# Kernel tuning notes

Measured on AMD Instinct MI355X. Metric: run time of the kernel, lower is better.

## Reference

```python
import jax, jax.numpy as jnp
import numpy as np

N_HEADS = 16
D_HEAD = 64
TAU = 30.0
NEG = -1e9


def setup_inputs() -> dict:
    key = jax.random.key(0)
    k1, k2, k3, k4 = jax.random.split(key, 4)
    B, L, D = 2, 2048, 1024
    scale = 1.0 / np.sqrt(D)
    return {
        "input": jax.random.normal(k1, (B, L, D), dtype=jnp.float32),
        "attention_mask": jnp.ones((B, L), dtype=jnp.int32),
        "W_Q": jax.random.normal(k2, (N_HEADS * D_HEAD, D), dtype=jnp.float32) * scale,
        "W_K": jax.random.normal(k3, (N_HEADS * D_HEAD, D), dtype=jnp.float32) * scale,
        "W_V": jax.random.normal(k4, (N_HEADS * D_HEAD, D), dtype=jnp.float32) * scale,
    }


def reference(input, attention_mask, W_Q, W_K, W_V):
    B, L, D = input.shape
    # fused QKV projection (F.linear: x @ W.T), split into heads: [B, H, L, Dh]
    def proj(W):
        return jnp.einsum('bld,ed->ble', input, W).reshape(B, L, N_HEADS, D_HEAD).transpose(0, 2, 1, 3)
    q, k, v = proj(W_Q), proj(W_K), proj(W_V)
    S = jnp.einsum('bhqd,bhkd->bhqk', q, k) / np.sqrt(D_HEAD)  # [B,H,L,L]
    S = TAU * jnp.tanh(S)
    causal = jnp.tril(jnp.ones((L, L), dtype=bool))            # True = keep
    keep = causal[None, None, :, :] & (attention_mask[:, None, None, :] != 0)
    S = jnp.where(keep, S, NEG)
    attn = jax.nn.softmax(S, axis=-1)
    out = jnp.einsum('bhqk,bhkd->bhqd', attn, v)
    return out.transpose(0, 2, 1, 3).reshape(B, L, N_HEADS * D_HEAD)
```

## Files before the change

kernel.cpp:

```cpp
#include <hip/hip_runtime.h>
#include <hip/hip_bf16.h>


typedef unsigned short u16;
typedef __bf16 bf16x8 __attribute__((ext_vector_type(8)));
typedef float f32x4 __attribute__((ext_vector_type(4)));

#define MFMA(a, b, c) __builtin_amdgcn_mfma_f32_16x16x32_bf16(a, b, c, 0, 0, 0)

__device__ __forceinline__ u16 bf16rne(float f) {
    unsigned int u = __float_as_uint(f);
    u += 0x7fffu + ((u >> 16) & 1u);
    return (u16)(u >> 16);
}
__device__ __forceinline__ float bf16f(u16 h) {
    return __uint_as_float(((unsigned int)h) << 16);
}
__device__ __forceinline__ void split1(float f, u16& hi, u16& lo) {
    hi = bf16rne(f);
    lo = bf16rne(f - bf16f(hi));
}
__device__ __forceinline__ unsigned int pk2(float a, float b) {
    __hip_bfloat162 t = __float22bfloat162_rn(float2{a, b});
    return *(unsigned int*)&t;
}

__device__ __forceinline__ void gl16(const u16* g, u16* l) {
    __builtin_amdgcn_global_load_lds(
        (const __attribute__((address_space(1))) unsigned int*)g,
        (__attribute__((address_space(3))) unsigned int*)l, 16, 0, 0);
}

__global__ __launch_bounds__(256) void presplit(
    const float* __restrict__ X, const float* __restrict__ Wq,
    const float* __restrict__ Wk, const float* __restrict__ Wv,
    u16* __restrict__ Xh, u16* __restrict__ Xl,
    u16* __restrict__ Wqh, u16* __restrict__ Wql,
    u16* __restrict__ Wkh, u16* __restrict__ Wkl,
    u16* __restrict__ Wvh)
{
    int i = blockIdx.x * 256 + threadIdx.x;
    const float* src; u16 *dh, *dl; int off;
    if (i < 1048576)      { src = X;  dh = Xh;  dl = Xl;      off = i; }
    else if (i < 1310720) { src = Wq; dh = Wqh; dl = Wql;     off = i - 1048576; }
    else if (i < 1572864) { src = Wk; dh = Wkh; dl = Wkl;     off = i - 1310720; }
    else                  { src = Wv; dh = Wvh; dl = nullptr; off = i - 1572864; }
    float4 v = ((const float4*)src)[off];
    ushort4 h, l;
    split1(v.x, h.x, l.x); split1(v.y, h.y, l.y);
    split1(v.z, h.z, l.z); split1(v.w, h.w, l.w);
    ((ushort4*)dh)[off] = h;
    if (dl) ((ushort4*)dl)[off] = l;
}

__global__ __launch_bounds__(256, 4) void qkv_gemm(
    const u16* __restrict__ Xh, const u16* __restrict__ Xl,
    const u16* __restrict__ Wqh, const u16* __restrict__ Wql,
    const u16* __restrict__ Wkh, const u16* __restrict__ Wkl,
    const u16* __restrict__ Wvh,
    u16* __restrict__ Qh, u16* __restrict__ Ql,
    u16* __restrict__ Kh, u16* __restrict__ Kl,
    u16* __restrict__ VT)
{
    __shared__ __align__(16) u16 S[16384];
    u16* const Xhs = &S[0];
    u16* const Xls = &S[4096];
    u16* const Whs = &S[8192];
    u16* const Wls = &S[12288];
    const int tid = threadIdx.x;
    const int wave = tid >> 6, lane = tid & 63, quad = lane >> 4, c16 = lane & 15;
    const int id = blockIdx.x;
    const int nb = (((id >> 3) % 3) << 3) | (id & 7);
    const int m0 = ((id >> 3) / 3) * 128;
    const int mat = nb >> 3;
    const int n0 = (nb & 7) * 128;
    const u16* Bh = (mat == 0) ? Wqh : ((mat == 1) ? Wkh : Wvh);
    const u16* Bl = (mat == 0) ? Wql : Wkl;
    const int nseg = (mat < 2) ? 3 : 1;
    const int wm = (wave >> 1) * 64, wn = (wave & 1) * 64;

    const int srow0 = wave * 32 + (lane >> 2), scol = (lane & 3) * 8;

    f32x4 acc[4][4];
#pragma unroll
    for (int i = 0; i < 4; i++)
#pragma unroll
        for (int j = 0; j < 4; j++) acc[i][j] = (f32x4){0.f, 0.f, 0.f, 0.f};

    for (int kt = 0; kt < 32; kt++) {
        const int kcol = kt * 32;
#pragma unroll
        for (int s = 0; s < 2; s++) {
            int row = srow0 + s * 16;
            size_t go = (size_t)row * 1024 + kcol + scol;
            int lo = row * 32 + scol;
            gl16(Xh + (size_t)m0 * 1024 + go, &Xhs[lo]);
            gl16(Bh + (size_t)n0 * 1024 + go, &Whs[lo]);
            if (nseg == 3) {
                gl16(Xl + (size_t)m0 * 1024 + go, &Xls[lo]);
                gl16(Bl + (size_t)n0 * 1024 + go, &Wls[lo]);
            }
        }
        __syncthreads();
        for (int seg = 0; seg < nseg; seg++) {
            const u16* ap = (seg < 2) ? Xhs : Xls;
            const u16* bp = (seg == 1) ? Wls : Whs;
            bf16x8 af[4], bfr[4];
#pragma unroll
            for (int mt = 0; mt < 4; mt++)
                af[mt] = *(const bf16x8*)&ap[(wm + mt * 16 + c16) * 32 + quad * 8];
#pragma unroll
            for (int nt = 0; nt < 4; nt++)
                bfr[nt] = *(const bf16x8*)&bp[(wn + nt * 16 + c16) * 32 + quad * 8];
#pragma unroll
            for (int mt = 0; mt < 4; mt++)
#pragma unroll
                for (int nt = 0; nt < 4; nt++)
                    acc[mt][nt] = MFMA(af[mt], bfr[nt], acc[mt][nt]);
        }
        __syncthreads();
    }

    if (mat == 2) {
        u16* const T2 = &S[wave * 4096];
        const int nglob = n0 + wn + lane;
        const int hh = nglob >> 6, dh = nglob & 63;
        const int bh64 = ((m0 >> 11) * 16 + hh) * 64 + dh;
        u16* const vrow = VT + (size_t)bh64 * 2048 + (m0 & 2047) + wm;
#pragma unroll
        for (int half = 0; half < 2; half++) {
#pragma unroll
            for (int mt2 = 0; mt2 < 2; mt2++) {
                int mt = half * 2 + mt2;
#pragma unroll
                for (int nt = 0; nt < 4; nt++) {
                    uint2 d;
                    d.x = pk2(acc[mt][nt][0], acc[mt][nt][1]);
                    d.y = pk2(acc[mt][nt][2], acc[mt][nt][3]);
                    *(uint2*)&T2[(nt * 16 + c16) * 40 + mt2 * 16 + quad * 4] = d;
                }
            }
#pragma unroll
            for (int c = 0; c < 4; c++) {
                uint4 d = *(const uint4*)&T2[lane * 40 + c * 8];
                *(uint4*)&vrow[half * 32 + c * 8] = d;
            }
        }
    } else {
        const float scale = (mat == 0) ? 0.125f : 1.f;
#pragma unroll
        for (int mt = 0; mt < 4; mt++) {
#pragma unroll
            for (int nt = 0; nt < 4; nt++) {
#pragma unroll
                for (int reg = 0; reg < 4; reg++) {
                    int mm = m0 + wm + mt * 16 + quad * 4 + reg;
                    int n = n0 + wn + nt * 16 + c16;
                    int b_ = mm >> 11, l = mm & 2047;
                    int h = n >> 6, dh = n & 63;
                    float v = acc[mt][nt][reg] * scale;
                    u16 hi, lo; split1(v, hi, lo);
                    int idx = ((b_ * 16 + h) * 2048 + l) * 64 + dh;
                    if (mat == 0) { Qh[idx] = hi; Ql[idx] = lo; }
                    else          { Kh[idx] = hi; Kl[idx] = lo; }
                }
            }
        }
    }
}

__global__ __launch_bounds__(256, 4) void attn(
    const u16* __restrict__ Qh, const u16* __restrict__ Ql,
    const u16* __restrict__ Kh, const u16* __restrict__ Kl,
    const u16* __restrict__ VT, const int* __restrict__ AM,
    u16* __restrict__ Op, float* __restrict__ Lp)
{
    __shared__ __align__(16) u16 Khs[2][4096];
    __shared__ __align__(16) u16 Kls[2][4096];
    __shared__ __align__(16) u16 Ps[4096];

    const int tid = threadIdx.x, wave = tid >> 6, lane = tid & 63;
    const int quad = lane >> 4, c16 = lane & 15;
    const int bh = blockIdx.x;
    const int pr = blockIdx.y;
    const int sp = blockIdx.z;
    const int b_ = bh >> 4;
    const size_t base = (size_t)bh * 2048 * 64;

    const int swsub[2] = { (wave * 2) >> 2, (wave * 2 + 1) >> 2 };
    const int swrow[2] = { ((wave * 2) & 3) * 16 + (lane >> 2), ((wave * 2 + 1) & 3) * 16 + (lane >> 2) };
    const int scol = (lane & 3) * 8;

    auto stageK = [&](int k0, int buf) {
        const u16* Kht = Kh + base + (size_t)k0 * 64;
        const u16* Klt = Kl + base + (size_t)k0 * 64;
#pragma unroll
        for (int s = 0; s < 2; s++) {
            int sub = swsub[s], row = swrow[s];
            int lo = sub * 2048 + row * 32 + scol;
            gl16(Kht + (size_t)row * 64 + sub * 32 + scol, &Khs[buf][lo]);
            gl16(Klt + (size_t)row * 64 + sub * 32 + scol, &Kls[buf][lo]);
        }
    };

    for (int tix = 0; tix < 2; ++tix) {
        const int qt = tix ? pr : 31 - pr;
        const int q0 = qt * 64;

        const size_t qrow = base + (size_t)(q0 + wave * 16 + c16) * 64 + quad * 8;
        bf16x8 qh0 = *(const bf16x8*)&Qh[qrow];
        bf16x8 qh1 = *(const bf16x8*)&Qh[qrow + 32];
        bf16x8 ql0 = *(const bf16x8*)&Ql[qrow];
        bf16x8 ql1 = *(const bf16x8*)&Ql[qrow + 32];

        float rsl[4] = {0.f, 0.f, 0.f, 0.f};
        f32x4 o[4];
#pragma unroll
        for (int r = 0; r < 4; r++) o[r] = (f32x4){0.f, 0.f, 0.f, 0.f};

        if (sp <= qt) {
            stageK(sp * 64, 0);
            int cur = 0;
            for (int kb = sp; kb <= qt; kb += 2) {
                const int k0 = kb * 64;
                __syncthreads();
                if (kb + 2 <= qt) stageK(k0 + 128, cur ^ 1);

                int mk[4];
#pragma unroll
                for (int nt = 0; nt < 4; nt++)
                    mk[nt] = AM[b_ * 2048 + k0 + nt * 16 + c16];
                bf16x8 vf[4][2];
#pragma unroll
                for (int dt = 0; dt < 4; dt++) {
                    const size_t vrow = (size_t)(bh * 64 + dt * 16 + c16) * 2048 + k0 + quad * 8;
                    vf[dt][0] = *(const bf16x8*)&VT[vrow];
                    vf[dt][1] = *(const bf16x8*)&VT[vrow + 32];
                }
                const bool interior = (kb < qt);

                float p[4][4];
#pragma unroll
                for (int nt = 0; nt < 4; nt++) {
                    bf16x8 kh0 = *(const bf16x8*)&Khs[cur][(nt * 16 + c16) * 32 + quad * 8];
                    bf16x8 kh1 = *(const bf16x8*)&Khs[cur][2048 + (nt * 16 + c16) * 32 + quad * 8];
                    bf16x8 kl0 = *(const bf16x8*)&Kls[cur][(nt * 16 + c16) * 32 + quad * 8];
                    bf16x8 kl1 = *(const bf16x8*)&Kls[cur][2048 + (nt * 16 + c16) * 32 + quad * 8];
                    f32x4 sa = (f32x4){0.f, 0.f, 0.f, 0.f};
                    sa = MFMA(qh0, kh0, sa);
                    sa = MFMA(qh1, kh1, sa);
                    sa = MFMA(ql0, kh0, sa);
                    sa = MFMA(ql1, kh1, sa);
                    sa = MFMA(qh0, kl0, sa);
                    sa = MFMA(qh1, kl1, sa);
                    const int key = k0 + nt * 16 + c16;
                    const bool mok = (mk[nt] != 0);
#pragma unroll
                    for (int reg = 0; reg < 4; reg++) {
                        int qg = q0 + wave * 16 + quad * 4 + reg;
                        float x = sa[reg];
                        float e1 = __expf(2.f * x);
                        float r  = __builtin_amdgcn_rcpf(e1 + 1.f);
                        float pv = __expf(-60.f * r);
                        bool keep = mok && (interior || key <= qg);
                        pv = keep ? pv : 0.f;
                        p[nt][reg] = pv;
                        rsl[reg] += pv;
                    }
                }

#pragma unroll
                for (int nt = 0; nt < 4; nt++) {
                    int kl_ = nt * 16 + c16, sub = kl_ >> 5, kc = kl_ & 31;
#pragma unroll
                    for (int reg = 0; reg < 4; reg++)
                        Ps[sub * 2048 + (wave * 16 + quad * 4 + reg) * 32 + kc] = bf16rne(p[nt][reg]);
                }
                bf16x8 p0 = *(const bf16x8*)&Ps[(wave * 16 + c16) * 32 + quad * 8];
                bf16x8 p1 = *(const bf16x8*)&Ps[2048 + (wave * 16 + c16) * 32 + quad * 8];
#pragma unroll
                for (int dt = 0; dt < 4; dt++) {
                    o[dt] = MFMA(p0, vf[dt][0], o[dt]);
                    o[dt] = MFMA(p1, vf[dt][1], o[dt]);
                }
                cur ^= 1;
            }
        }
        __syncthreads();

        const size_t obase = (((size_t)sp * 1024 + (size_t)bh * 32 + qt) * 4096);
        const size_t lbase = (((size_t)sp * 1024 + (size_t)bh * 32 + qt) * 64);
        float lsum[4];
#pragma unroll
        for (int reg = 0; reg < 4; reg++) {
            float v = rsl[reg];
#pragma unroll
            for (int off = 1; off < 16; off <<= 1)
                v += __shfl_xor(v, off);
            lsum[reg] = v;
        }
        if (c16 == 0) {
#pragma unroll
            for (int reg = 0; reg < 4; reg++)
                Lp[lbase + wave * 16 + quad * 4 + reg] = lsum[reg];
        }
#pragma unroll
        for (int dt = 0; dt < 4; dt++)
#pragma unroll
            for (int reg = 0; reg < 4; reg++) {
                int row = wave * 16 + quad * 4 + reg;
                int d = dt * 16 + c16;
                Op[obase + row * 64 + d] = bf16rne(o[dt][reg]);
            }
    }
}

__global__ __launch_bounds__(256) void combine(
    const u16* __restrict__ Op, const float* __restrict__ Lp,
    float* __restrict__ Out)
{
    const int i = blockIdx.x * 256 + threadIdx.x;
    const size_t lin = (size_t)i * 4;
    const int d  = (int)(lin & 1023);
    const int h  = d >> 6, dd = d & 63;
    const int l  = (int)((lin >> 10) & 2047);
    const int b  = (int)(lin >> 21);
    const int qt = l >> 6, row = l & 63;
    const int bh = b * 16 + h;
    const size_t o0 = (((size_t)bh * 32 + qt) * 4096) + row * 64 + dd;
    const size_t o1 = o0 + (size_t)1024 * 4096;
    const size_t l0 = (((size_t)bh * 32 + qt) * 64) + row;
    ushort4 pa = *(const ushort4*)&Op[o0];
    ushort4 pb = *(const ushort4*)&Op[o1];
    float inv = __builtin_amdgcn_rcpf(Lp[l0] + Lp[l0 + 65536]);
    float4 r;
    r.x = (bf16f(pa.x) + bf16f(pb.x)) * inv;
    r.y = (bf16f(pa.y) + bf16f(pb.y)) * inv;
    r.z = (bf16f(pa.z) + bf16f(pb.z)) * inv;
    r.w = (bf16f(pa.w) + bf16f(pb.w)) * inv;
    *(float4*)&Out[lin] = r;
}

extern "C" void kernel_launch(void* const* d_in, const int* in_sizes, int n_in,
                              void* d_out, int out_size, void* d_ws, size_t ws_size,
                              hipStream_t stream) {
    const float* X  = (const float*)d_in[0];
    const int*   AM = (const int*)d_in[1];
    const float* Wq = (const float*)d_in[2];
    const float* Wk = (const float*)d_in[3];
    const float* Wv = (const float*)d_in[4];
    float* out = (float*)d_out;

    const size_t NE = (size_t)2 * 16 * 2048 * 64;
    const size_t WN = (size_t)1024 * 1024;
    u16* Qh  = (u16*)d_ws;
    u16* Ql  = Qh + NE;
    u16* Kh  = Ql + NE;
    u16* Kl  = Kh + NE;
    u16* VT  = Kl + NE;
    u16* Xh  = VT + NE;
    u16* Xl  = Xh + NE;
    u16* Wqh = Xl + NE;
    u16* Wql = Wqh + WN;
    u16* Wkh = Wql + WN;
    u16* Wkl = Wkh + WN;
    u16* Wvh = Wkl + WN;
    u16*   Op = Xh;
    float* Lp = (float*)Wqh;

    presplit<<<7168, 256, 0, stream>>>(X, Wq, Wk, Wv, Xh, Xl, Wqh, Wql, Wkh, Wkl, Wvh);
    qkv_gemm<<<768, 256, 0, stream>>>(Xh, Xl, Wqh, Wql, Wkh, Wkl, Wvh,
                                      Qh, Ql, Kh, Kl, VT);
    attn<<<dim3(32, 16, 2), 256, 0, stream>>>(Qh, Ql, Kh, Kl, VT, AM, Op, Lp);
    combine<<<4096, 256, 0, stream>>>(Op, Lp, out);
}
```

Measured before the change: 242.7 us.

## Transpose QK^T MFMA so P stays in registers and skip LDS round-trip

The attention kernel swaps the MFMA operand order so each lane holds scores for one query across four consecutive keys. That lets the P tile be packed straight into bf16x8 registers for the PV MFMA, removing the Ps shared-memory write/read and the per-row 16-lane shuffle reduction. V loads are split into two 4-element halves to match the new key ordering. The exponentials now use exp2 with log2e folded into the Q scale and the tanh constant, and the mask is read as int4. The QKV GEMM reorders its split-bf16 MFMA segments to reuse loaded fragments and lowers its occupancy hint from 4 to 3, which changes the register budget.

```diff
diff --git a/kernel.cpp b/kernel.cpp
--- a/kernel.cpp
+++ b/kernel.cpp
@@ -4,6 +4,7 @@
 
 typedef unsigned short u16;
 typedef __bf16 bf16x8 __attribute__((ext_vector_type(8)));
+typedef __bf16 bf16x4 __attribute__((ext_vector_type(4)));
 typedef float f32x4 __attribute__((ext_vector_type(4)));
 
 #define MFMA(a, b, c) __builtin_amdgcn_mfma_f32_16x16x32_bf16(a, b, c, 0, 0, 0)
@@ -23,6 +24,13 @@
 __device__ __forceinline__ unsigned int pk2(float a, float b) {
     __hip_bfloat162 t = __float22bfloat162_rn(float2{a, b});
     return *(unsigned int*)&t;
+}
+__device__ __forceinline__ float fexp2(float x) {
+#if __has_builtin(__builtin_amdgcn_exp2f)
+    return __builtin_amdgcn_exp2f(x);
+#else
+    return __expf(x * 0.6931471805599453f);
+#endif
 }
 
 __device__ __forceinline__ void gl16(const u16* g, u16* l) {
@@ -53,7 +61,7 @@
     if (dl) ((ushort4*)dl)[off] = l;
 }
 
-__global__ __launch_bounds__(256, 4) void qkv_gemm(
+__global__ __launch_bounds__(256, 3) void qkv_gemm(
     const u16* __restrict__ Xh, const u16* __restrict__ Xl,
     const u16* __restrict__ Wqh, const u16* __restrict__ Wql,
     const u16* __restrict__ Wkh, const u16* __restrict__ Wkl,
@@ -102,21 +110,37 @@
             }
         }
         __syncthreads();
-        for (int seg = 0; seg < nseg; seg++) {
-            const u16* ap = (seg < 2) ? Xhs : Xls;
-            const u16* bp = (seg == 1) ? Wls : Whs;
-            bf16x8 af[4], bfr[4];
+        bf16x8 xh[4], wh[4];
+#pragma unroll
+        for (int mt = 0; mt < 4; mt++)
+            xh[mt] = *(const bf16x8*)&Xhs[(wm + mt * 16 + c16) * 32 + quad * 8];
+#pragma unroll
+        for (int nt = 0; nt < 4; nt++)
+            wh[nt] = *(const bf16x8*)&Whs[(wn + nt * 16 + c16) * 32 + quad * 8];
+#pragma unroll
+        for (int mt = 0; mt < 4; mt++)
+#pragma unroll
+            for (int nt = 0; nt < 4; nt++)
+                acc[mt][nt] = MFMA(xh[mt], wh[nt], acc[mt][nt]);
+        if (nseg == 3) {
+            bf16x8 wl[4];
+#pragma unroll
+            for (int nt = 0; nt < 4; nt++)
+                wl[nt] = *(const bf16x8*)&Wls[(wn + nt * 16 + c16) * 32 + quad * 8];
 #pragma unroll
             for (int mt = 0; mt < 4; mt++)
-                af[mt] = *(const bf16x8*)&ap[(wm + mt * 16 + c16) * 32 + quad * 8];
-#pragma unroll
-            for (int nt = 0; nt < 4; nt++)
-                bfr[nt] = *(const bf16x8*)&bp[(wn + nt * 16 + c16) * 32 + quad * 8];
+#pragma unroll
+                for (int nt = 0; nt < 4; nt++)
+                    acc[mt][nt] = MFMA(xh[mt], wl[nt], acc[mt][nt]);
+            bf16x8 xl[4];
 #pragma unroll
             for (int mt = 0; mt < 4; mt++)
+                xl[mt] = *(const bf16x8*)&Xls[(wm + mt * 16 + c16) * 32 + quad * 8];
+#pragma unroll
+            for (int mt = 0; mt < 4; mt++)
 #pragma unroll
                 for (int nt = 0; nt < 4; nt++)
-                    acc[mt][nt] = MFMA(af[mt], bfr[nt], acc[mt][nt]);
+                    acc[mt][nt] = MFMA(xl[mt], wh[nt], acc[mt][nt]);
         }
         __syncthreads();
     }
@@ -147,7 +171,7 @@
             }
         }
     } else {
-        const float scale = (mat == 0) ? 0.125f : 1.f;
+        const float scale = (mat == 0) ? 0.36067376022224085f : 1.f;
 #pragma unroll
         for (int mt = 0; mt < 4; mt++) {
 #pragma unroll
@@ -177,7 +201,6 @@
 {
     __shared__ __align__(16) u16 Khs[2][4096];
     __shared__ __align__(16) u16 Kls[2][4096];
-    __shared__ __align__(16) u16 Ps[4096];
 
     const int tid = threadIdx.x, wave = tid >> 6, lane = tid & 63;
     const int quad = lane >> 4, c16 = lane & 15;
@@ -203,6 +226,8 @@
         }
     };
 
+    union U8 { uint4 u; bf16x8 v; };
+
     for (int tix = 0; tix < 2; ++tix) {
         const int qt = tix ? pr : 31 - pr;
         const int q0 = qt * 64;
@@ -213,7 +238,7 @@
         bf16x8 ql0 = *(const bf16x8*)&Ql[qrow];
         bf16x8 ql1 = *(const bf16x8*)&Ql[qrow + 32];
 
-        float rsl[4] = {0.f, 0.f, 0.f, 0.f};
+        float rsl = 0.f;
         f32x4 o[4];
 #pragma unroll
         for (int r = 0; r < 4; r++) o[r] = (f32x4){0.f, 0.f, 0.f, 0.f};
@@ -221,21 +246,26 @@
         if (sp <= qt) {
             stageK(sp * 64, 0);
             int cur = 0;
+            const int qg = q0 + wave * 16 + c16;
             for (int kb = sp; kb <= qt; kb += 2) {
                 const int k0 = kb * 64;
                 __syncthreads();
                 if (kb + 2 <= qt) stageK(k0 + 128, cur ^ 1);
 
-                int mk[4];
+                int4 mk[4];
 #pragma unroll
                 for (int nt = 0; nt < 4; nt++)
-                    mk[nt] = AM[b_ * 2048 + k0 + nt * 16 + c16];
-                bf16x8 vf[4][2];
+                    mk[nt] = *(const int4*)&AM[b_ * 2048 + k0 + nt * 16 + quad * 4];
+                bf16x4 vlo[4][2], vhi[4][2];
 #pragma unroll
                 for (int dt = 0; dt < 4; dt++) {
-                    const size_t vrow = (size_t)(bh * 64 + dt * 16 + c16) * 2048 + k0 + quad * 8;
-                    vf[dt][0] = *(const bf16x8*)&VT[vrow];
-                    vf[dt][1] = *(const bf16x8*)&VT[vrow + 32];
+#pragma unroll
+                    for (int hf = 0; hf < 2; hf++) {
+                        const size_t vb = (size_t)(bh * 64 + dt * 16 + c16) * 2048
+                                        + k0 + hf * 32 + quad * 4;
+                        vlo[dt][hf] = *(const bf16x4*)&VT[vb];
+                        vhi[dt][hf] = *(const bf16x4*)&VT[vb + 16];
+                    }
                 }
                 const bool interior = (kb < qt);
 
@@ -247,41 +277,39 @@
                     bf16x8 kl0 = *(const bf16x8*)&Kls[cur][(nt * 16 + c16) * 32 + quad * 8];
                     bf16x8 kl1 = *(const bf16x8*)&Kls[cur][2048 + (nt * 16 + c16) * 32 + quad * 8];
                     f32x4 sa = (f32x4){0.f, 0.f, 0.f, 0.f};
-                    sa = MFMA(qh0, kh0, sa);
-                    sa = MFMA(qh1, kh1, sa);
-                    sa = MFMA(ql0, kh0, sa);
-                    sa = MFMA(ql1, kh1, sa);
-                    sa = MFMA(qh0, kl0, sa);
-                    sa = MFMA(qh1, kl1, sa);
-                    const int key = k0 + nt * 16 + c16;
-                    const bool mok = (mk[nt] != 0);
+                    sa = MFMA(kh0, qh0, sa);
+                    sa = MFMA(kh1, qh1, sa);
+                    sa = MFMA(kl0, qh0, sa);
+                    sa = MFMA(kl1, qh1, sa);
+                    sa = MFMA(kh0, ql0, sa);
+                    sa = MFMA(kh1, ql1, sa);
+                    const int kbase = k0 + nt * 16 + quad * 4;
+                    const int mm[4] = { mk[nt].x, mk[nt].y, mk[nt].z, mk[nt].w };
 #pragma unroll
                     for (int reg = 0; reg < 4; reg++) {
-                        int qg = q0 + wave * 16 + quad * 4 + reg;
-                        float x = sa[reg];
-                        float e1 = __expf(2.f * x);
+                        float e1 = fexp2(sa[reg]);
                         float r  = __builtin_amdgcn_rcpf(e1 + 1.f);
-                        float pv = __expf(-60.f * r);
-                        bool keep = mok && (interior || key <= qg);
+                        float pv = fexp2(-86.561702453337804f * r);
+                        bool keep = (mm[reg] != 0) && (interior || (kbase + reg) <= qg);
                         pv = keep ? pv : 0.f;
                         p[nt][reg] = pv;
-                        rsl[reg] += pv;
+                        rsl += pv;
                     }
                 }
 
-#pragma unroll
-                for (int nt = 0; nt < 4; nt++) {
-                    int kl_ = nt * 16 + c16, sub = kl_ >> 5, kc = kl_ & 31;
-#pragma unroll
-                    for (int reg = 0; reg < 4; reg++)
-                        Ps[sub * 2048 + (wave * 16 + quad * 4 + reg) * 32 + kc] = bf16rne(p[nt][reg]);
-                }
-                bf16x8 p0 = *(const bf16x8*)&Ps[(wave * 16 + c16) * 32 + quad * 8];
-                bf16x8 p1 = *(const bf16x8*)&Ps[2048 + (wave * 16 + c16) * 32 + quad * 8];
+                U8 pa0, pa1;
+                pa0.u.x = pk2(p[0][0], p[0][1]); pa0.u.y = pk2(p[0][2], p[0][3]);
+                pa0.u.z = pk2(p[1][0], p[1][1]); pa0.u.w = pk2(p[1][2], p[1][3]);
+                pa1.u.x = pk2(p[2][0], p[2][1]); pa1.u.y = pk2(p[2][2], p[2][3]);
+                pa1.u.z = pk2(p[3][0], p[3][1]); pa1.u.w = pk2(p[3][2], p[3][3]);
 #pragma unroll
                 for (int dt = 0; dt < 4; dt++) {
-                    o[dt] = MFMA(p0, vf[dt][0], o[dt]);
-                    o[dt] = MFMA(p1, vf[dt][1], o[dt]);
+                    bf16x8 v0 = __builtin_shufflevector(vlo[dt][0], vhi[dt][0],
+                                                        0, 1, 2, 3, 4, 5, 6, 7);
+                    bf16x8 v1 = __builtin_shufflevector(vlo[dt][1], vhi[dt][1],
+                                                        0, 1, 2, 3, 4, 5, 6, 7);
+                    o[dt] = MFMA(pa0.v, v0, o[dt]);
+                    o[dt] = MFMA(pa1.v, v1, o[dt]);
                 }
                 cur ^= 1;
             }
@@ -290,20 +318,11 @@
 
         const size_t obase = (((size_t)sp * 1024 + (size_t)bh * 32 + qt) * 4096);
         const size_t lbase = (((size_t)sp * 1024 + (size_t)bh * 32 + qt) * 64);
-        float lsum[4];
-#pragma unroll
-        for (int reg = 0; reg < 4; reg++) {
-            float v = rsl[reg];
-#pragma unroll
-            for (int off = 1; off < 16; off <<= 1)
-                v += __shfl_xor(v, off);
-            lsum[reg] = v;
-        }
-        if (c16 == 0) {
-#pragma unroll
-            for (int reg = 0; reg < 4; reg++)
-                Lp[lbase + wave * 16 + quad * 4 + reg] = lsum[reg];
-        }
+        float v = rsl;
+        v += __shfl_xor(v, 16);
+        v += __shfl_xor(v, 32);
+        if (quad == 0)
+            Lp[lbase + wave * 16 + c16] = v;
 #pragma unroll
         for (int dt = 0; dt < 4; dt++)
 #pragma unroll
```

After: 287.5 us. 18.5% more time.
